# Optimization experiments

Hardware: AMD Instinct MI355X
Metric: run time of the kernel (lower is better)

The kernel has to match this reference:

```python
import math
import jax, jax.numpy as jnp
import numpy as np

B, S, D_IN = 2, 2048, 1024
DKQ, DV, H = 1024, 1024, 16
HEAD_SIZE = DKQ / H  # attention_head_size (float division, as in torch)


def setup_inputs() -> dict:
    key = jax.random.key(0)
    k1, k2, k3, k4, k5, k6 = jax.random.split(key, 6)
    std = 1.0 / math.sqrt(D_IN)
    return {
        'hidden_states': jax.random.normal(k1, (B, S, D_IN), dtype=jnp.float32),
        'Wq': jax.random.normal(k2, (DKQ, D_IN), dtype=jnp.float32) * std,
        'Wk': jax.random.normal(k3, (DKQ, D_IN), dtype=jnp.float32) * std,
        'Wv': jax.random.normal(k4, (DV, D_IN), dtype=jnp.float32) * std,
        'bv': jax.random.normal(k5, (DV,), dtype=jnp.float32) * std,
        'mixing': jax.random.normal(k6, (H, DKQ), dtype=jnp.float32) * 0.2,  # UNIFORM init: normal(std=0.2)
    }


def reference(hidden_states, Wq, Wk, Wv, bv, mixing):
    # Q, K: [B, S, DKQ]; V: [B, S, DV]
    q = jnp.einsum('bsd,ed->bse', hidden_states, Wq)
    k = jnp.einsum('bsd,ed->bse', hidden_states, Wk)
    v = jnp.einsum('bsd,ed->bse', hidden_states, Wv) + bv
    # per-head query mixing: mixed_q[b,h,s,e] = q[b,s,e] * mixing[h,e]
    # scores[b,h,s,t] = sum_e mixed_q[b,h,s,e] * k[b,t,e]
    scores = jnp.einsum('bse,he,bte->bhst', q, mixing, k)
    scores = scores / math.sqrt(HEAD_SIZE)
    probs = jax.nn.softmax(scores, axis=-1)
    # value heads: [B, H, S, DV/H]
    v_h = v.reshape(v.shape[0], v.shape[1], H, DV // H).transpose(0, 2, 1, 3)
    ctx = jnp.einsum('bhst,bhtd->bhsd', probs, v_h)
    # back to [B, S, DV]
    ctx = ctx.transpose(0, 2, 1, 3).reshape(hidden_states.shape[0], hidden_states.shape[1], DV)
    return ctx
```

## Files before the change

kernel.cpp:

```cpp
#include <hip/hip_runtime.h>

#define B_ 2
#define S_ 2048
#define D_ 1024
#define H_ 16
#define HD_ 64

typedef _Float16 f16;
typedef _Float16 half8 __attribute__((ext_vector_type(8)));
typedef float float4_ __attribute__((ext_vector_type(4)));

#define N_HS (B_*S_*D_)
#define N_W  (D_*D_)
#define N_MIX (H_*D_)

__device__ __forceinline__ void gl_lds16(const f16* g, const f16* l) {
  __builtin_amdgcn_global_load_lds(
      (const __attribute__((address_space(1))) void*)g,
      (__attribute__((address_space(3))) void*)l, 16, 0, 0);
}

#define MIX_SCALE 0.18033688011112042f

__global__ __launch_bounds__(256) void convert_kernel(
    const float* __restrict__ hs, const float* __restrict__ wq,
    const float* __restrict__ wk, const float* __restrict__ wv,
    const float* __restrict__ mix,
    f16* __restrict__ hs16, f16* __restrict__ wq16, f16* __restrict__ wk16,
    f16* __restrict__ wv16, f16* __restrict__ mix16)
{
  const int total4 = (N_HS + 3*N_W + N_MIX) / 4;
  for (int i4 = blockIdx.x*blockDim.x + threadIdx.x; i4 < total4;
       i4 += gridDim.x*blockDim.x) {
    int i = i4*4;
    const float* src; f16* dst; float scale = 1.0f; int off;
    if (i < N_HS)            { src=hs;  dst=hs16;  off=i; }
    else if (i < N_HS+N_W)   { src=wq;  dst=wq16;  off=i-N_HS; }
    else if (i < N_HS+2*N_W) { src=wk;  dst=wk16;  off=i-N_HS-N_W; }
    else if (i < N_HS+3*N_W) { src=wv;  dst=wv16;  off=i-N_HS-2*N_W; }
    else                     { src=mix; dst=mix16; off=i-N_HS-3*N_W; scale=MIX_SCALE; }
    float4 v = *(const float4*)(src+off);
    dst[off]   = (f16)(v.x*scale);
    dst[off+1] = (f16)(v.y*scale);
    dst[off+2] = (f16)(v.z*scale);
    dst[off+3] = (f16)(v.w*scale);
  }
}

#define BM 128
#define BN 128
#define BK 64
#define LDC 136

__global__ __launch_bounds__(256, 2) void qkv_kernel(
    const f16* __restrict__ hs16, const f16* __restrict__ w16base,
    const float* __restrict__ bv,
    f16* __restrict__ q16, f16* __restrict__ k16, f16* __restrict__ vT)
{
  const int z = blockIdx.z;
  const f16* W = w16base + (size_t)z * N_W;
  f16* out = (z==0) ? q16 : k16;
  const int mt = blockIdx.y, nt = blockIdx.x;
  const int tid = threadIdx.x;
  const int lane = tid & 63, wid = tid >> 6;
  const int wm = wid >> 1, wn = wid & 1;
  const int quad = lane >> 4, l16 = lane & 15;

  __shared__ __align__(16) union {
    struct { f16 As[BM*BK]; f16 Bs[BN*BK]; } s;
    f16 Cs[BM*LDC];
  } u;

  float4_ acc[4][4];
#pragma unroll
  for (int i=0;i<4;i++)
#pragma unroll
    for (int j=0;j<4;j++) acc[i][j] = (float4_)0.0f;

  const int row0 = mt*BM;
  const int col0 = nt*BN;

  for (int ko = 0; ko < D_; ko += BK) {
#pragma unroll
    for (int c=0; c<4; c++) {
      int slot = (wid*4+c)*64 + lane;
      int r = slot >> 3;
      int gc = (slot & 7) ^ (r & 7);
      gl_lds16(hs16 + (size_t)(row0+r)*D_ + ko + gc*8, u.s.As + (size_t)(wid*4+c)*64*8);
      gl_lds16(W    + (size_t)(col0+r)*D_ + ko + gc*8, u.s.Bs + (size_t)(wid*4+c)*64*8);
    }
    __syncthreads();
#pragma unroll
    for (int kk=0; kk<BK; kk+=32) {
      int ck = (kk >> 3) + quad;
      half8 a[4], b[4];
#pragma unroll
      for (int i=0;i<4;i++) {
        int rr = wm*64 + i*16 + l16;
        a[i] = *(const half8*)&u.s.As[(size_t)(((rr<<3) | (ck ^ (rr&7))) << 3)];
      }
#pragma unroll
      for (int j=0;j<4;j++) {
        int rr = wn*64 + j*16 + l16;
        b[j] = *(const half8*)&u.s.Bs[(size_t)(((rr<<3) | (ck ^ (rr&7))) << 3)];
      }
#pragma unroll
      for (int i=0;i<4;i++)
#pragma unroll
        for (int j=0;j<4;j++)
          acc[i][j] = __builtin_amdgcn_mfma_f32_16x16x32_f16(a[i], b[j], acc[i][j], 0,0,0);
    }
    __syncthreads();
  }

#pragma unroll
  for (int i=0;i<4;i++) {
#pragma unroll
    for (int j=0;j<4;j++) {
      int c = wn*64 + j*16 + l16;
      float bias = (z==2) ? bv[col0 + c] : 0.0f;
#pragma unroll
      for (int r=0;r<4;r++) {
        int rr = wm*64 + i*16 + quad*4 + r;
        f16 val = (f16)(acc[i][j][r] + bias);
        u.Cs[(z==2) ? ((size_t)c*LDC + rr) : ((size_t)rr*LDC + c)] = val;
      }
    }
  }
  __syncthreads();
  {
    const int c = tid >> 1, half = tid & 1;
    const f16* srcp = &u.Cs[(size_t)c*LDC + half*64];
    f16* dst;
    if (z == 2) {
      int bb = row0 >> 11, ss0 = (row0 & (S_-1)) + half*64;
      dst = vT + ((size_t)bb*D_ + col0 + c)*S_ + ss0;
    } else {
      dst = out + (size_t)(row0 + c)*D_ + col0 + half*64;
    }
#pragma unroll
    for (int k=0;k<8;k++)
      *(float4*)(dst + k*8) = *(const float4*)(srcp + k*8);
  }
}

#define TQ 128
#define TK 128
#define LDA 72
#define LDP 136

__global__ __launch_bounds__(256, 2) void attn_kernel(
    const f16* __restrict__ q16, const f16* __restrict__ k16,
    const f16* __restrict__ vT, const f16* __restrict__ mix16,
    float* __restrict__ out)
{
  const int b = blockIdx.z;
  const int h = blockIdx.y;
  const int s0 = blockIdx.x * TQ;
  const int tid = threadIdx.x;
  const int lane = tid & 63, wid = tid >> 6;
  const int wm = wid >> 1, wn = wid & 1;
  const int quad = lane >> 4, l16 = lane & 15;

  __shared__ __align__(16) union {
    struct { f16 q[TQ][LDA]; f16 k0[TK*BK]; f16 k1[TK*BK]; } s1;
    f16 P[TQ][LDP];
  } u;
  __shared__ __align__(16) float red_l[2][TQ];

  float l_lane[16];
#pragma unroll
  for (int t=0;t<16;t++) l_lane[t] = 0.0f;

  float4_ o_acc[4][2];
#pragma unroll
  for (int i=0;i<4;i++)
#pragma unroll
    for (int j=0;j<2;j++) o_acc[i][j] = (float4_)0.0f;

  const f16* qbase = q16 + (size_t)(b*S_ + s0)*D_;
  const f16* kbase = k16 + (size_t)b*S_*D_;
  const f16* mrow  = mix16 + h*D_;
  const f16* vTb   = vT + (size_t)(b*D_ + h*HD_)*S_;

  for (int t0 = 0; t0 < S_; t0 += 2*TK) {
    float4_ sacc[2][4][4];
#pragma unroll
    for (int tt=0;tt<2;tt++)
#pragma unroll
      for (int i=0;i<4;i++)
#pragma unroll
        for (int j=0;j<4;j++) sacc[tt][i][j] = (float4_)0.0f;

    for (int ko = 0; ko < D_; ko += BK) {
      const f16* k0g = kbase + (size_t)t0*D_ + ko;
      const f16* k1g = k0g + (size_t)TK*D_;
#pragma unroll
      for (int c=0; c<4; c++) {
        int slot = (wid*4+c)*64 + lane;
        int r = slot >> 3;
        int gc = (slot & 7) ^ (r & 7);
        gl_lds16(k0g + (size_t)r*D_ + gc*8, u.s1.k0 + (size_t)(wid*4+c)*64*8);
        gl_lds16(k1g + (size_t)r*D_ + gc*8, u.s1.k1 + (size_t)(wid*4+c)*64*8);
      }
#pragma unroll
      for (int it=0; it<4; it++) {
        int c = it*256 + tid;
        int r = c >> 3, c8 = (c & 7)*8;
        half8 qv = *(const half8*)&qbase[(size_t)r*D_ + ko + c8];
        half8 mv = *(const half8*)&mrow[ko + c8];
        *(half8*)&u.s1.q[r][c8] = qv * mv;
      }
      __syncthreads();
      __builtin_amdgcn_s_setprio(1);
#pragma unroll
      for (int kk=0; kk<BK; kk+=32) {
        half8 a[4];
#pragma unroll
        for (int i=0;i<4;i++) a[i] = *(const half8*)&u.s1.q[wm*64+i*16+l16][kk+quad*8];
#pragma unroll
        for (int tt=0;tt<2;tt++) {
          const f16* kb = tt ? u.s1.k1 : u.s1.k0;
          half8 bf[4];
#pragma unroll
          for (int j=0;j<4;j++) {
            int rr = wn*64 + j*16 + l16;
            int ck = (kk >> 3) + quad;
            bf[j] = *(const half8*)&kb[(size_t)(((rr<<3) | (ck ^ (rr&7))) << 3)];
          }
#pragma unroll
          for (int i=0;i<4;i++)
#pragma unroll
            for (int j=0;j<4;j++)
              sacc[tt][i][j] = __builtin_amdgcn_mfma_f32_16x16x32_f16(a[i], bf[j], sacc[tt][i][j], 0,0,0);
        }
      }
      __builtin_amdgcn_s_setprio(0);
      __syncthreads();
    }

#pragma unroll
    for (int tt=0;tt<2;tt++) {
#pragma unroll
      for (int i=0;i<4;i++)
#pragma unroll
        for (int j=0;j<4;j++)
#pragma unroll
          for (int r=0;r<4;r++) {
            float p = __builtin_exp2f(sacc[tt][i][j][r]);
            l_lane[i*4+r] += p;
            u.P[wm*64+i*16+quad*4+r][wn*64+j*16+l16] = (f16)p;
          }

      half8 vb[8];
#pragma unroll
      for (int ki=0; ki<4; ki++)
#pragma unroll
        for (int j=0; j<2; j++) {
          int ch = wn*32 + j*16 + l16;
          vb[ki*2+j] = *(const half8*)&vTb[(size_t)ch*S_ + t0 + tt*TK + ki*32 + quad*8];
        }

      __syncthreads();

      __builtin_amdgcn_s_setprio(1);
#pragma unroll
      for (int ki=0; ki<4; ki++) {
        half8 pa[4];
#pragma unroll
        for (int i=0;i<4;i++) pa[i] = *(const half8*)&u.P[wm*64+i*16+l16][ki*32+quad*8];
#pragma unroll
        for (int i=0;i<4;i++)
#pragma unroll
          for (int j=0;j<2;j++)
            o_acc[i][j] = __builtin_amdgcn_mfma_f32_16x16x32_f16(vb[ki*2+j], pa[i], o_acc[i][j], 0,0,0);
      }
      __builtin_amdgcn_s_setprio(0);
      __syncthreads();
    }
  }

#pragma unroll
  for (int d=1; d<16; d<<=1)
#pragma unroll
    for (int t=0;t<16;t++) l_lane[t] += __shfl_xor(l_lane[t], d);
  if (l16 == 0) {
#pragma unroll
    for (int i=0;i<4;i++)
#pragma unroll
      for (int r=0;r<4;r++)
        red_l[wn][wm*64+i*16+quad*4+r] = l_lane[i*4+r];
  }
  __syncthreads();

#pragma unroll
  for (int i=0;i<4;i++) {
    int row = wm*64 + i*16 + l16;
    float linv = 1.0f / (red_l[0][row] + red_l[1][row]);
#pragma unroll
    for (int j=0;j<2;j++) {
      float4 v4;
      v4.x = o_acc[i][j][0] * linv;
      v4.y = o_acc[i][j][1] * linv;
      v4.z = o_acc[i][j][2] * linv;
      v4.w = o_acc[i][j][3] * linv;
      *(float4*)&out[(size_t)(b*S_ + s0 + row)*D_ + h*HD_ + wn*32 + j*16 + quad*4] = v4;
    }
  }
}

extern "C" void kernel_launch(void* const* d_in, const int* in_sizes, int n_in,
                              void* d_out, int out_size, void* d_ws, size_t ws_size,
                              hipStream_t stream) {
  (void)in_sizes; (void)n_in; (void)out_size; (void)ws_size;
  const float* hs  = (const float*)d_in[0];
  const float* Wq  = (const float*)d_in[1];
  const float* Wk  = (const float*)d_in[2];
  const float* Wv  = (const float*)d_in[3];
  const float* bv  = (const float*)d_in[4];
  const float* mix = (const float*)d_in[5];
  float* out = (float*)d_out;

  char* ws = (char*)d_ws;
  f16* hs16  = (f16*)(ws);
  f16* w16   = (f16*)(ws + 8388608);
  f16* mix16 = (f16*)(ws + 14680064);
  f16* q16   = (f16*)(ws + 14712832);
  f16* k16   = (f16*)(ws + 23101440);
  f16* vT    = (f16*)(ws + 31490048);

  convert_kernel<<<2048, 256, 0, stream>>>(hs, Wq, Wk, Wv, mix,
                                           hs16, w16, w16+N_W, w16+2*N_W, mix16);
  qkv_kernel<<<dim3(D_/BN, (B_*S_)/BM, 3), 256, 0, stream>>>(
      hs16, w16, bv, q16, k16, vT);
  attn_kernel<<<dim3(S_/TQ, H_, B_), 256, 0, stream>>>(
      q16, k16, vT, mix16, out);
}
```

Baseline: 407.0 us.

## Double-buffer K tiles in attention QK loop with manual waitcnt barriers

Restructures the QK^T reduction loop so the next K chunk pair is prefetched into a second LDS buffer via global_load_lds while the current one feeds the MFMAs. Full __syncthreads are replaced by explicit vmcnt/lgkmcnt waits and raw s_barrier. Q staging is XOR-swizzled, and red_l is folded into the shared union to keep the LDS footprint compatible with two blocks per CU. The aim is to hide global load latency behind compute, at the cost of fragile hand-tuned waitcnt counts and extra LDS for the doubled K buffers.

```diff
diff --git a/kernel.cpp b/kernel.cpp
--- a/kernel.cpp
+++ b/kernel.cpp
@@ -19,6 +19,10 @@
       (const __attribute__((address_space(1))) void*)g,
       (__attribute__((address_space(3))) void*)l, 16, 0, 0);
 }
+
+#define VM_WAIT8()  asm volatile("s_waitcnt vmcnt(8)" ::: "memory")
+#define LGKM0()     asm volatile("s_waitcnt lgkmcnt(0)" ::: "memory")
+#define RAW_BAR()   asm volatile("s_barrier" ::: "memory")
 
 #define MIX_SCALE 0.18033688011112042f
 
@@ -146,7 +150,6 @@
 
 #define TQ 128
 #define TK 128
-#define LDA 72
 #define LDP 136
 
 __global__ __launch_bounds__(256, 2) void attn_kernel(
@@ -163,10 +166,10 @@
   const int quad = lane >> 4, l16 = lane & 15;
 
   __shared__ __align__(16) union {
-    struct { f16 q[TQ][LDA]; f16 k0[TK*BK]; f16 k1[TK*BK]; } s1;
-    f16 P[TQ][LDP];
+    struct { f16 k[4][TK*BK]; f16 q[TQ*BK]; } s;
+    struct { f16 _pad[2*TK*BK]; f16 P[TQ][LDP]; } p;
+    struct { float red_l[2][TQ]; } r;
   } u;
-  __shared__ __align__(16) float red_l[2][TQ];
 
   float l_lane[16];
 #pragma unroll
@@ -183,7 +186,35 @@
   const f16* mrow  = mix16 + h*D_;
   const f16* vTb   = vT + (size_t)(b*D_ + h*HD_)*S_;
 
+#define STAGE_PAIR(pr, t0g, ko_) do {                                        \
+    const f16* k0g_ = kbase + (size_t)(t0g)*D_ + (ko_);                      \
+    const f16* k1g_ = k0g_ + (size_t)TK*D_;                                  \
+    _Pragma("unroll")                                                        \
+    for (int c_=0; c_<4; c_++) {                                             \
+      int slot_ = (wid*4+c_)*64 + lane;                                      \
+      int r_ = slot_ >> 3;                                                   \
+      int gc_ = (slot_ & 7) ^ (r_ & 7);                                      \
+      gl_lds16(k0g_ + (size_t)r_*D_ + gc_*8, u.s.k[2*(pr)]   + (size_t)(wid*4+c_)*64*8); \
+      gl_lds16(k1g_ + (size_t)r_*D_ + gc_*8, u.s.k[2*(pr)+1] + (size_t)(wid*4+c_)*64*8); \
+    } } while (0)
+
+#define QSTAGE(ko_) do {                                                     \
+    _Pragma("unroll")                                                        \
+    for (int it_=0; it_<4; it_++) {                                          \
+      int c_ = it_*256 + tid; int r_ = c_>>3; int cc_ = c_&7;                \
+      half8 qv_ = *(const half8*)&qbase[(size_t)r_*D_ + (ko_) + cc_*8];      \
+      half8 mv_ = *(const half8*)&mrow[(ko_) + cc_*8];                       \
+      *(half8*)&u.s.q[(size_t)(((r_<<3) | (cc_ ^ (r_&7))) << 3)] = qv_ * mv_; \
+    } } while (0)
+
+  STAGE_PAIR(0, 0, 0);
+
   for (int t0 = 0; t0 < S_; t0 += 2*TK) {
+    const bool has_next = (t0 + 2*TK < S_);
+
+    QSTAGE(0);
+    STAGE_PAIR(1, t0, BK);
+
     float4_ sacc[2][4][4];
 #pragma unroll
     for (int tt=0;tt<2;tt++)
@@ -192,40 +223,32 @@
 #pragma unroll
         for (int j=0;j<4;j++) sacc[tt][i][j] = (float4_)0.0f;
 
-    for (int ko = 0; ko < D_; ko += BK) {
-      const f16* k0g = kbase + (size_t)t0*D_ + ko;
-      const f16* k1g = k0g + (size_t)TK*D_;
-#pragma unroll
-      for (int c=0; c<4; c++) {
-        int slot = (wid*4+c)*64 + lane;
-        int r = slot >> 3;
-        int gc = (slot & 7) ^ (r & 7);
-        gl_lds16(k0g + (size_t)r*D_ + gc*8, u.s1.k0 + (size_t)(wid*4+c)*64*8);
-        gl_lds16(k1g + (size_t)r*D_ + gc*8, u.s1.k1 + (size_t)(wid*4+c)*64*8);
-      }
-#pragma unroll
-      for (int it=0; it<4; it++) {
-        int c = it*256 + tid;
-        int r = c >> 3, c8 = (c & 7)*8;
-        half8 qv = *(const half8*)&qbase[(size_t)r*D_ + ko + c8];
-        half8 mv = *(const half8*)&mrow[ko + c8];
-        *(half8*)&u.s1.q[r][c8] = qv * mv;
-      }
-      __syncthreads();
+#pragma unroll 2
+    for (int ko_i = 0; ko_i < D_/BK; ko_i++) {
+      const int ko = ko_i * BK;
+      const int cur = ko_i & 1;
+
+      VM_WAIT8();
+      LGKM0();
+      RAW_BAR();
+
       __builtin_amdgcn_s_setprio(1);
 #pragma unroll
-      for (int kk=0; kk<BK; kk+=32) {
+      for (int kk2=0; kk2<2; kk2++) {
+        const int ck = kk2*4 + quad;
         half8 a[4];
 #pragma unroll
-        for (int i=0;i<4;i++) a[i] = *(const half8*)&u.s1.q[wm*64+i*16+l16][kk+quad*8];
+        for (int i=0;i<4;i++) {
+          int rr = wm*64 + i*16 + l16;
+          a[i] = *(const half8*)&u.s.q[(size_t)(((rr<<3) | (ck ^ (rr&7))) << 3)];
+        }
 #pragma unroll
         for (int tt=0;tt<2;tt++) {
-          const f16* kb = tt ? u.s1.k1 : u.s1.k0;
+          const f16* kb = u.s.k[2*cur + tt];
           half8 bf[4];
 #pragma unroll
           for (int j=0;j<4;j++) {
             int rr = wn*64 + j*16 + l16;
-            int ck = (kk >> 3) + quad;
             bf[j] = *(const half8*)&kb[(size_t)(((rr<<3) | (ck ^ (rr&7))) << 3)];
           }
 #pragma unroll
@@ -236,7 +259,16 @@
         }
       }
       __builtin_amdgcn_s_setprio(0);
-      __syncthreads();
+
+      RAW_BAR();
+
+      if (ko_i < 14) {
+        QSTAGE(ko + BK);
+        STAGE_PAIR(cur, t0, ko + 2*BK);
+      } else if (ko_i == 14) {
+        QSTAGE(ko + BK);
+        if (has_next) STAGE_PAIR(0, t0 + 2*TK, 0);
+      }
     }
 
 #pragma unroll
@@ -249,7 +281,7 @@
           for (int r=0;r<4;r++) {
             float p = __builtin_exp2f(sacc[tt][i][j][r]);
             l_lane[i*4+r] += p;
-            u.P[wm*64+i*16+quad*4+r][wn*64+j*16+l16] = (f16)p;
+            u.p.P[wm*64+i*16+quad*4+r][wn*64+j*16+l16] = (f16)p;
           }
 
       half8 vb[8];
@@ -261,14 +293,15 @@
           vb[ki*2+j] = *(const half8*)&vTb[(size_t)ch*S_ + t0 + tt*TK + ki*32 + quad*8];
         }
 
-      __syncthreads();
+      LGKM0();
+      RAW_BAR();
 
       __builtin_amdgcn_s_setprio(1);
 #pragma unroll
       for (int ki=0; ki<4; ki++) {
         half8 pa[4];
 #pragma unroll
-        for (int i=0;i<4;i++) pa[i] = *(const half8*)&u.P[wm*64+i*16+l16][ki*32+quad*8];
+        for (int i=0;i<4;i++) pa[i] = *(const half8*)&u.p.P[wm*64+i*16+l16][ki*32+quad*8];
 #pragma unroll
         for (int i=0;i<4;i++)
 #pragma unroll
@@ -276,7 +309,7 @@
             o_acc[i][j] = __builtin_amdgcn_mfma_f32_16x16x32_f16(vb[ki*2+j], pa[i], o_acc[i][j], 0,0,0);
       }
       __builtin_amdgcn_s_setprio(0);
-      __syncthreads();
+      RAW_BAR();
     }
   }
 
@@ -289,14 +322,14 @@
     for (int i=0;i<4;i++)
 #pragma unroll
       for (int r=0;r<4;r++)
-        red_l[wn][wm*64+i*16+quad*4+r] = l_lane[i*4+r];
+        u.r.red_l[wn][wm*64+i*16+quad*4+r] = l_lane[i*4+r];
   }
   __syncthreads();
 
 #pragma unroll
   for (int i=0;i<4;i++) {
     int row = wm*64 + i*16 + l16;
-    float linv = 1.0f / (red_l[0][row] + red_l[1][row]);
+    float linv = 1.0f / (u.r.red_l[0][row] + u.r.red_l[1][row]);
 #pragma unroll
     for (int j=0;j<2;j++) {
       float4 v4;
```

After: 761.7 us. 87.2% more time.
